# Optimization experiments

Measured on AMD Instinct MI355X. Metric: run time of the kernel, lower is better.

## Reference

```python
import jax, jax.numpy as jnp
import numpy as np

B, H, K, HID = 64, 32, 4096, 7168
Q_LORA, KV_LORA = 1536, 512
NOPE, ROPE, VDIM = 128, 64, 128
HEAD_SIZE = NOPE + ROPE  # 192
EPS = 1e-6
SOFTMAX_SCALE = HEAD_SIZE ** -0.5  # mscale = 1 (no yarn)


def rmsnorm(x, w, eps=EPS):
    return x * jax.lax.rsqrt(jnp.mean(x * x, axis=-1, keepdims=True) + eps) * w


def interleave_rope(x, cos, sin):
    # x: [..., ROPE]; replicate torch view(d//2,2).transpose(2,3).reshape(d):
    # interleaved [r0,i0,r1,i1,...] -> [r0,r1,...,i0,i1,...], then rotate-half RoPE.
    shp = x.shape
    x = jnp.swapaxes(x.reshape(shp[:-1] + (ROPE // 2, 2)), -1, -2).reshape(shp)
    x1, x2 = x[..., : ROPE // 2], x[..., ROPE // 2:]
    # cos/sin: [B, ROPE//2] -> broadcast over head axis
    c = cos[:, None, :]
    s = sin[:, None, :]
    return jnp.concatenate([x1 * c - x2 * s, x2 * c + x1 * s], axis=-1)


def setup_inputs() -> dict:
    key = jax.random.key(0)
    ks = jax.random.split(key, 12)
    w = 0.02
    return {
        "hidden_states": jax.random.normal(ks[0], (B, HID), jnp.float32),
        "cos": jax.random.uniform(ks[1], (B, ROPE // 2), jnp.float32),
        "sin": jax.random.uniform(ks[2], (B, ROPE // 2), jnp.float32),
        "kv_cache": jax.random.normal(ks[3], (B, K, KV_LORA + ROPE), jnp.float32),
        "w_q_a": jax.random.normal(ks[4], (HID, Q_LORA), jnp.float32) * w,
        "q_a_ln_w": jnp.ones((Q_LORA,), jnp.float32),
        "w_q_b": jax.random.normal(ks[5], (Q_LORA, H * HEAD_SIZE), jnp.float32) * w,
        "w_kv_a": jax.random.normal(ks[6], (HID, KV_LORA + ROPE), jnp.float32) * w,
        "kv_a_ln_w": jnp.ones((KV_LORA,), jnp.float32),
        "w_uk_t": jax.random.normal(ks[7], (H, NOPE, KV_LORA), jnp.float32) * w,
        "w_uv": jax.random.normal(ks[8], (H, KV_LORA, VDIM), jnp.float32) * w,
        "w_o": jax.random.normal(ks[9], (H * VDIM, HID), jnp.float32) * w,
        "slots": jnp.full((B,), K - 1, jnp.int32),
        "seq_lens": jnp.full((B,), K, jnp.int32),
    }


def reference(hidden_states, cos, sin, kv_cache, w_q_a, q_a_ln_w, w_q_b,
              w_kv_a, kv_a_ln_w, w_uk_t, w_uv, w_o, slots, seq_lens):
    # --- Q low-rank path: q_a_proj -> RMSNorm -> q_b_proj ---
    q_c = rmsnorm(hidden_states @ w_q_a, q_a_ln_w)          # [B, Q_LORA]
    q = (q_c @ w_q_b).reshape(B, H, HEAD_SIZE)              # [B, H, 192]
    q_nope, q_pe = q[..., :NOPE], q[..., NOPE:]

    # --- K-up absorption: ql_nope = q_nope @ W_UK_T (per head) ---
    ql_nope = jnp.einsum("bhn,hnr->bhr", q_nope, w_uk_t)    # [B, H, KV_LORA]

    # --- compressed KV projection ---
    ckv = hidden_states @ w_kv_a                            # [B, KV_LORA+ROPE]
    kv_c, k_pe = ckv[:, :KV_LORA], ckv[:, KV_LORA:]
    kv_c = rmsnorm(kv_c, kv_a_ln_w)                         # [B, KV_LORA]
    k_pe = k_pe[:, None, :]                                 # [B, 1, ROPE]

    # --- interleaved RoPE on pe parts ---
    q_pe = interleave_rope(q_pe, cos, sin)                  # [B, H, ROPE]
    k_pe = interleave_rope(k_pe, cos, sin)[:, 0, :]         # [B, ROPE]

    # --- latent cache writeback ---
    latent_k = jnp.concatenate([kv_c, k_pe], axis=-1)       # [B, KV_LORA+ROPE]
    cache = kv_cache.at[jnp.arange(B), slots].set(latent_k)  # [B, K, 576]

    # --- MLA latent attention (decode) ---
    query = jnp.concatenate([ql_nope, q_pe], axis=-1)       # [B, H, 576]
    scores = jnp.einsum("bhd,bkd->bhk", query, cache) * SOFTMAX_SCALE
    valid = (jnp.arange(K)[None, :] < seq_lens[:, None])[:, None, :]  # [B,1,K]
    scores = jnp.where(valid, scores, jnp.finfo(scores.dtype).min)
    probs = jax.nn.softmax(scores, axis=-1)                 # [B, H, K]
    attn = jnp.einsum("bhk,bkr->bhr", probs, cache[..., :KV_LORA])  # [B,H,KV_LORA]

    # --- V-up absorption + output projection ---
    out = jnp.einsum("bhr,hrv->bhv", attn, w_uv)            # [B, H, VDIM]
    return out.reshape(B, H * VDIM) @ w_o                   # [B, HID]
```

## Files before the change

### kernel.cpp

```cpp
#include <hip/hip_runtime.h>
#include <stdint.h>

#define NB 64
#define NH 32
#define KCTX 4096
#define HID 7168
#define QLORA 1536
#define KVL 512
#define DTOT 576
#define NSPLIT 4
#define KSPAN 1024
#define NTILE 64
#define TK 16
#define SM_SCALE 0.07216878364870323f
#define NEGINF (-3.0e38f)

typedef __attribute__((ext_vector_type(4))) float f32x4;
typedef __attribute__((ext_vector_type(8))) __bf16 bf16x8;

#define LGKM_BARRIER() do{ asm volatile("s_waitcnt lgkmcnt(0)" ::: "memory"); __builtin_amdgcn_s_barrier(); } while(0)

static __device__ __forceinline__ void glds16(const void* g, void* s){
    __builtin_amdgcn_global_load_lds((const __attribute__((address_space(1))) void*)g,
                                     (__attribute__((address_space(3))) void*)s, 16, 0, 0);
}

static __device__ __forceinline__ unsigned short f2bf(float f){
    union{__bf16 h; unsigned short s;} x; x.h = (__bf16)f; return x.s;
}
static __device__ __forceinline__ float bf2f(unsigned short h){
    union{unsigned i;float f;}x; x.i=((unsigned)h)<<16; return x.f;
}
static __device__ __forceinline__ unsigned pack2(float a, float b){
    union{__bf16 h[2]; unsigned u;} x; x.h[0]=(__bf16)a; x.h[1]=(__bf16)b; return x.u;
}

__global__ __launch_bounds__(256) void pack_a(const float* __restrict__ A,
        unsigned short* __restrict__ Hi, unsigned short* __restrict__ Lo, int K)
{
    int idx = blockIdx.x*256 + threadIdx.x;
    int m = idx & 63, kb = idx >> 6;
    const float* src = A + (size_t)m*K + kb*8;
    float v[8];
    *(float4*)(v)   = *(const float4*)(src);
    *(float4*)(v+4) = *(const float4*)(src+4);
    unsigned short h[8], l[8];
#pragma unroll
    for (int j=0;j<8;++j){
        h[j] = f2bf(v[j]);
        l[j] = f2bf(v[j] - bf2f(h[j]));
    }
    uint4 uh, ul;
    uh.x=(unsigned)h[0]|((unsigned)h[1]<<16); uh.y=(unsigned)h[2]|((unsigned)h[3]<<16);
    uh.z=(unsigned)h[4]|((unsigned)h[5]<<16); uh.w=(unsigned)h[6]|((unsigned)h[7]<<16);
    ul.x=(unsigned)l[0]|((unsigned)l[1]<<16); ul.y=(unsigned)l[2]|((unsigned)l[3]<<16);
    ul.z=(unsigned)l[4]|((unsigned)l[5]<<16); ul.w=(unsigned)l[6]|((unsigned)l[7]<<16);
    *(uint4*)(Hi + (size_t)idx*8) = uh;
    *(uint4*)(Lo + (size_t)idx*8) = ul;
}

static __device__ __forceinline__ void gemm_core(
        const unsigned short* __restrict__ Ahi, const unsigned short* __restrict__ Alo,
        const float* __restrict__ Wm, float* __restrict__ P, int N, int ksteps,
        int bx, int by,
        unsigned short* Ah, unsigned short* Al, unsigned short* Bh, unsigned short* Bl)
{
    const int tid = threadIdx.x;
    const int w = tid>>6, l = tid&63, lm = l&15, lg = l>>4;
    const int n0 = bx*64;
    const int s  = by;
    const int mn = tid&63, ks = tid>>6;
    const int widx = ((mn>>4)*64 + ks*16 + (mn&15));

    f32x4 acc[4];
#pragma unroll
    for (int i=0;i<4;++i){ acc[i][0]=0.f; acc[i][1]=0.f; acc[i][2]=0.f; acc[i][3]=0.f; }

    uint4 ah4, al4; float wv[8];
    auto load_raw = [&](int t){
        const int k0 = (s*ksteps + t)*32;
        size_t gidx = (size_t)((k0>>3) + ks)*64 + mn;
        ah4 = *(const uint4*)(Ahi + gidx*8);
        al4 = *(const uint4*)(Alo + gidx*8);
        const float* wp = Wm + (size_t)(k0 + ks*8)*N + n0 + mn;
#pragma unroll
        for (int j=0;j<8;++j) wv[j] = wp[(size_t)j*N];
    };
    auto cvt_write = [&](int buf){
        unsigned short h[8], lo[8];
#pragma unroll
        for (int j=0;j<8;++j){
            h[j]  = f2bf(wv[j]);
            lo[j] = f2bf(wv[j] - bf2f(h[j]));
        }
        uint4 bh4, bl4;
        bh4.x=(unsigned)h[0]|((unsigned)h[1]<<16); bh4.y=(unsigned)h[2]|((unsigned)h[3]<<16);
        bh4.z=(unsigned)h[4]|((unsigned)h[5]<<16); bh4.w=(unsigned)h[6]|((unsigned)h[7]<<16);
        bl4.x=(unsigned)lo[0]|((unsigned)lo[1]<<16); bl4.y=(unsigned)lo[2]|((unsigned)lo[3]<<16);
        bl4.z=(unsigned)lo[4]|((unsigned)lo[5]<<16); bl4.w=(unsigned)lo[6]|((unsigned)lo[7]<<16);
        *(uint4*)(Ah + buf*2048 + widx*8) = ah4;
        *(uint4*)(Al + buf*2048 + widx*8) = al4;
        *(uint4*)(Bh + buf*2048 + widx*8) = bh4;
        *(uint4*)(Bl + buf*2048 + widx*8) = bl4;
    };

    load_raw(0);
    for (int t=0; t<ksteps; ++t){
        const int buf = t&1;
        cvt_write(buf);
        __syncthreads();
        if (t+1 < ksteps) load_raw(t+1);
        const int fa = buf*2048 + (w*64 + lg*16 + lm)*8;
        bf16x8 fah = *(const bf16x8*)(Ah + fa);
        bf16x8 fal = *(const bf16x8*)(Al + fa);
#pragma unroll
        for (int nt=0;nt<4;++nt){
            const int fb = buf*2048 + (nt*64 + lg*16 + lm)*8;
            bf16x8 fbh = *(const bf16x8*)(Bh + fb);
            bf16x8 fbl = *(const bf16x8*)(Bl + fb);
            acc[nt] = __builtin_amdgcn_mfma_f32_16x16x32_bf16(fah, fbh, acc[nt], 0,0,0);
            acc[nt] = __builtin_amdgcn_mfma_f32_16x16x32_bf16(fal, fbh, acc[nt], 0,0,0);
            acc[nt] = __builtin_amdgcn_mfma_f32_16x16x32_bf16(fah, fbl, acc[nt], 0,0,0);
        }
        __syncthreads();
    }
#pragma unroll
    for (int nt=0;nt<4;++nt){
        int n = n0 + nt*16 + lm;
#pragma unroll
        for (int r=0;r<4;++r){
            int m = w*16 + lg*4 + r;
            P[((size_t)s*64 + m)*N + n] = acc[nt][r];
        }
    }
}

__global__ __launch_bounds__(256) void gemm_mfma(
        const unsigned short* __restrict__ Ahi, const unsigned short* __restrict__ Alo,
        const float* __restrict__ Wm, float* __restrict__ P, int N, int ksteps)
{
    __shared__ unsigned short Ah[2*2048], Al[2*2048], Bh[2*2048], Bl[2*2048];
    gemm_core(Ahi, Alo, Wm, P, N, ksteps, blockIdx.x, blockIdx.y, Ah, Al, Bh, Bl);
}

__global__ __launch_bounds__(256) void gemm_dual(
        const unsigned short* __restrict__ Ahi, const unsigned short* __restrict__ Alo,
        const float* __restrict__ W0, float* __restrict__ P0, int N0, int ks0, int nbx0, int nblk0,
        const float* __restrict__ W1, float* __restrict__ P1, int N1, int ks1, int nbx1)
{
    __shared__ unsigned short Ah[2*2048], Al[2*2048], Bh[2*2048], Bl[2*2048];
    int bid = blockIdx.x;
    if (bid < nblk0){
        gemm_core(Ahi, Alo, W0, P0, N0, ks0, bid%nbx0, bid/nbx0, Ah, Al, Bh, Bl);
    } else {
        bid -= nblk0;
        gemm_core(Ahi, Alo, W1, P1, N1, ks1, bid%nbx1, bid/nbx1, Ah, Al, Bh, Bl);
    }
}

static __device__ __forceinline__ void rms_core(const float* __restrict__ P,
        const float* __restrict__ w, unsigned short* __restrict__ Hi,
        unsigned short* __restrict__ Lo, int S, int b, float* red)
{
    const int t = threadIdx.x;
    float v[6]; float ss = 0.f;
#pragma unroll
    for (int j=0;j<6;++j){
        int n = j*256 + t;
        float s = 0.f;
        for (int sp=0; sp<S; ++sp) s += P[((size_t)sp*64+b)*1536 + n];
        v[j] = s; ss += s*s;
    }
#pragma unroll
    for (int off=32; off>=1; off>>=1) ss += __shfl_xor(ss, off, 64);
    if ((t&63)==0) red[t>>6] = ss;
    __syncthreads();
    float tot = red[0]+red[1]+red[2]+red[3];
    float rs = rsqrtf(tot/1536.f + 1e-6f);
#pragma unroll
    for (int j=0;j<6;++j){
        int n = j*256+t;
        float val = v[j]*rs*w[n];
        unsigned short hs = f2bf(val);
        unsigned short ls = f2bf(val - bf2f(hs));
        size_t ui = (size_t)(n>>3)*512 + b*8 + (n&7);
        Hi[ui] = hs; Lo[ui] = ls;
    }
}

static __device__ __forceinline__ void kvrope_core(const float* __restrict__ P,
        const float* __restrict__ w, const float* __restrict__ cosb, const float* __restrict__ sinb,
        float* __restrict__ latent, int S, int b, float* vals, float* red)
{
    const int t = threadIdx.x;
    float ss = 0.f;
    for (int j=0;j<3;++j){
        int n = j*256+t;
        if (n < 576){
            float s=0.f;
            for (int sp=0;sp<S;++sp) s += P[((size_t)sp*64+b)*576 + n];
            vals[n]=s;
            if (n<512) ss += s*s;
        }
    }
#pragma unroll
    for (int off=32; off>=1; off>>=1) ss += __shfl_xor(ss, off, 64);
    if ((t&63)==0) red[t>>6]=ss;
    __syncthreads();
    float tot = red[0]+red[1]+red[2]+red[3];
    float rs = rsqrtf(tot/512.f + 1e-6f);
    for (int j=0;j<3;++j){
        int n = j*256+t;
        if (n<576){
            float o;
            if (n < 512) o = vals[n]*rs*w[n];
            else if (n < 544){ int i=n-512; o = vals[512+2*i]*cosb[b*32+i] - vals[513+2*i]*sinb[b*32+i]; }
            else            { int i=n-544; o = vals[513+2*i]*cosb[b*32+i] + vals[512+2*i]*sinb[b*32+i]; }
            latent[(size_t)b*576 + n] = o;
        }
    }
}

__global__ __launch_bounds__(256) void norm_dual(
        const float* __restrict__ Pq, const float* __restrict__ qw,
        unsigned short* __restrict__ Hi, unsigned short* __restrict__ Lo, int Sq,
        const float* __restrict__ Pkv, const float* __restrict__ kvw,
        const float* __restrict__ cosb, const float* __restrict__ sinb,
        float* __restrict__ latent, int Skv)
{
    __shared__ float vals[576];
    __shared__ float red[4];
    if (blockIdx.x < 64) rms_core(Pq, qw, Hi, Lo, Sq, blockIdx.x, red);
    else                 kvrope_core(Pkv, kvw, cosb, sinb, latent, Skv, blockIdx.x-64, vals, red);
}

__global__ __launch_bounds__(256) void reduce_sum(const float* __restrict__ P,
        float* __restrict__ out, int S, int N)
{
    int i = blockIdx.x*256 + threadIdx.x;
    int b = i / N, n = i - b*N;
    float s = 0.f;
    for (int sp=0; sp<S; ++sp) s += P[((size_t)sp*64+b)*N + n];
    out[i] = s;
}

__global__ __launch_bounds__(256) void finish_q(const float* __restrict__ P,
        const float* __restrict__ cosb, const float* __restrict__ sinb,
        float* __restrict__ q, float* __restrict__ query, int S)
{
    int i = blockIdx.x*256 + threadIdx.x;
    int b = i / 6144, n = i - b*6144;
    float s = 0.f;
    for (int sp=0; sp<S; ++sp) s += P[((size_t)sp*64+b)*6144 + n];
    int h = n/192, nl = n - h*192;
    if (nl < 128){
        q[((size_t)b*32+h)*192 + nl] = s;
    } else {
        int i2 = (nl-128)>>1;
        float other = __shfl_xor(s, 1);
        float c = cosb[b*32+i2], sn = sinb[b*32+i2];
        float* o = query + ((size_t)b*32+h)*576;
        if ((nl&1)==0) o[512+i2] = s*c - other*sn;
        else           o[544+i2] = s*c + other*sn;
    }
}

__global__ __launch_bounds__(256) void qlnope_mfma(const float* __restrict__ q,
        const float* __restrict__ wukt, float* __restrict__ query)
{
    __shared__ unsigned short Bh[4096], Bl[4096];
    const int h = blockIdx.x, r0 = blockIdx.y*128;
    const int tid = threadIdx.x;
    const int w = tid>>6, l = tid&63, lm = l&15, lg = l>>4;
    f32x4 acc[8];
#pragma unroll
    for (int i=0;i<8;++i){ acc[i][0]=0.f; acc[i][1]=0.f; acc[i][2]=0.f; acc[i][3]=0.f; }

    for (int ck=0; ck<4; ++ck){
        const int k0 = ck*32;
        unsigned short hh[2][8], ll[2][8]; int wid0 = tid*2;
#pragma unroll
        for (int wi=0; wi<2; ++wi){
            int wid = wid0 + wi;
            int ntile = wid>>6, kg = (wid>>4)&3, nl = wid&15;
            int n = r0 + ntile*16 + nl;
            const float* wp = wukt + (size_t)h*65536 + (size_t)(k0+kg*8)*512 + n;
#pragma unroll
            for (int j=0;j<8;++j){
                float v = wp[(size_t)j*512];
                hh[wi][j] = f2bf(v);
                ll[wi][j] = f2bf(v - bf2f(hh[wi][j]));
            }
        }
        __syncthreads();
#pragma unroll
        for (int wi=0; wi<2; ++wi){
            int wid = wid0 + wi;
            uint4 uh, ul;
            uh.x=(unsigned)hh[wi][0]|((unsigned)hh[wi][1]<<16); uh.y=(unsigned)hh[wi][2]|((unsigned)hh[wi][3]<<16);
            uh.z=(unsigned)hh[wi][4]|((unsigned)hh[wi][5]<<16); uh.w=(unsigned)hh[wi][6]|((unsigned)hh[wi][7]<<16);
            ul.x=(unsigned)ll[wi][0]|((unsigned)ll[wi][1]<<16); ul.y=(unsigned)ll[wi][2]|((unsigned)ll[wi][3]<<16);
            ul.z=(unsigned)ll[wi][4]|((unsigned)ll[wi][5]<<16); ul.w=(unsigned)ll[wi][6]|((unsigned)ll[wi][7]<<16);
            *(uint4*)(Bh + wid*8) = uh;
            *(uint4*)(Bl + wid*8) = ul;
        }
        __syncthreads();
        const int bb = w*16 + lm;
        const float* ap = q + ((size_t)bb*32 + h)*192 + k0 + lg*8;
        float4 a0 = *(const float4*)ap;
        float4 a1 = *(const float4*)(ap+4);
        union{uint4 u; bf16x8 v;} fh, fl;
        fh.u.x=pack2(a0.x,a0.y); fh.u.y=pack2(a0.z,a0.w);
        fh.u.z=pack2(a1.x,a1.y); fh.u.w=pack2(a1.z,a1.w);
        float r0f=a0.x-bf2f(f2bf(a0.x)), r1f=a0.y-bf2f(f2bf(a0.y));
        float r2f=a0.z-bf2f(f2bf(a0.z)), r3f=a0.w-bf2f(f2bf(a0.w));
        float r4f=a1.x-bf2f(f2bf(a1.x)), r5f=a1.y-bf2f(f2bf(a1.y));
        float r6f=a1.z-bf2f(f2bf(a1.z)), r7f=a1.w-bf2f(f2bf(a1.w));
        fl.u.x=pack2(r0f,r1f); fl.u.y=pack2(r2f,r3f);
        fl.u.z=pack2(r4f,r5f); fl.u.w=pack2(r6f,r7f);
#pragma unroll
        for (int nt=0;nt<8;++nt){
            const int fb = (nt*64 + lg*16 + lm)*8;
            bf16x8 fbh = *(const bf16x8*)(Bh + fb);
            bf16x8 fbl = *(const bf16x8*)(Bl + fb);
            acc[nt] = __builtin_amdgcn_mfma_f32_16x16x32_bf16(fh.v, fbh, acc[nt], 0,0,0);
            acc[nt] = __builtin_amdgcn_mfma_f32_16x16x32_bf16(fl.v, fbh, acc[nt], 0,0,0);
            acc[nt] = __builtin_amdgcn_mfma_f32_16x16x32_bf16(fh.v, fbl, acc[nt], 0,0,0);
        }
        __syncthreads();
    }
#pragma unroll
    for (int nt=0;nt<8;++nt){
        int r = r0 + nt*16 + lm;
#pragma unroll
        for (int qq=0;qq<4;++qq){
            int bb = w*16 + lg*4 + qq;
            query[((size_t)bb*32 + h)*576 + r] = acc[nt][qq];
        }
    }
}

static __device__ __forceinline__ int vt_addr(int d, int key){
    return (d>>2)*64 + (((d&3)^((d>>3)&3))<<4) + key;
}

__global__ __launch_bounds__(512,1) void attn_mfma(const float* __restrict__ query,
        const float* __restrict__ kv, const float* __restrict__ latent,
        const int* __restrict__ slots, const int* __restrict__ seq_lens,
        float* __restrict__ Opart, float* __restrict__ Mpart, float* __restrict__ Lpart)
{
    __shared__ float Kf[3][16*576];
    __shared__ unsigned short Vt[8192];
    __shared__ float S_s[4][32][16];
    __shared__ unsigned short P_s[32][40];
    __shared__ float alpha_s[32];

    const int b = blockIdx.y, sp = blockIdx.x;
    const int tid = threadIdx.x;
    const int w = tid>>6, l = tid&63;
    const int lm = l&15, lg = l>>4;
    const int ht = w&1;
    const int dg = w>>1;
    const int cs = dg*5 - (dg>0?1:0);
    const int cnt = (dg==1||dg==2)?5:4;
    const int seqlen = seq_lens[b];
    const int slot = slots[b];
    const int k0 = sp*KSPAN;
    const int myh = tid>>4, s5 = tid&15;

    P_s[tid>>4][16 + (tid&15)] = 0;

    bf16x8 qf[5];
    {
        const float* qrow = query + ((size_t)b*32 + ht*16 + lm)*576;
#pragma unroll
        for (int ss=0;ss<5;++ss){
            if (ss < cnt){
                int d0 = (cs+ss)*32 + lg*8;
                float4 a = *(const float4*)(qrow + d0);
                float4 c = *(const float4*)(qrow + d0 + 4);
                union{uint4 u; bf16x8 v;} cv;
                cv.u.x=pack2(a.x,a.y); cv.u.y=pack2(a.z,a.w);
                cv.u.z=pack2(c.x,c.y); cv.u.w=pack2(c.z,c.w);
                qf[ss]=cv.v;
            } else {
                union{uint4 u; bf16x8 v;} z; z.u.x=0; z.u.y=0; z.u.z=0; z.u.w=0;
                qf[ss]=z.v;
            }
        }
    }

    auto issue_tile = [&](int tt, int buf){
        const int gkb = k0 + tt*TK;
#pragma unroll
        for (int i=0;i<5;++i){
            int s = i*8 + w;
            if (s < 36){
                int B = s*1024 + l*16;
                int r = B / 2304;
                int gs = (B - r*2304) >> 4;
                int g  = gs ^ (r&7);
                int gk = gkb + r; if (gk > KCTX-1) gk = KCTX-1;
                const float* src = (gk==slot) ? (latent + (size_t)b*576 + g*4)
                                              : (kv + ((size_t)b*KCTX + gk)*576 + g*4);
                glds16(src, ((char*)&Kf[buf][0]) + B);
            }
        }
    };

    f32x4 oacc[8];
#pragma unroll
    for (int i=0;i<8;++i){ oacc[i][0]=0.f; oacc[i][1]=0.f; oacc[i][2]=0.f; oacc[i][3]=0.f; }
    float m_run = NEGINF, l_run = 0.f;

    issue_tile(0, 0);
    issue_tile(1, 1);
    if (w < 4) { asm volatile("s_waitcnt vmcnt(5)" ::: "memory"); }
    else       { asm volatile("s_waitcnt vmcnt(4)" ::: "memory"); }
    __builtin_amdgcn_s_barrier();

    int cur = 0;
    for (int tt=0; tt<NTILE; ++tt){
        if (tt+2 < NTILE){
            int ib = cur+2; if (ib>=3) ib-=3;
            issue_tile(tt+2, ib);
        }

        {
            const int kg = tid&1;
            const int dq = (tid>>1)&127;
            const int rep = tid>>8;
            float4 rv[4];
#pragma unroll
            for (int i=0;i<4;++i){
                int r = kg*8 + rep*4 + i;
                rv[i] = *(const float4*)(&Kf[cur][r*576 + ((dq ^ (r&7))<<2)]);
            }
#pragma unroll
            for (int j=0;j<4;++j){
                uint2 o;
                o.x = pack2(((const float*)&rv[0])[j], ((const float*)&rv[1])[j]);
                o.y = pack2(((const float*)&rv[2])[j], ((const float*)&rv[3])[j]);
                *(uint2*)(Vt + vt_addr(dq*4+j, kg*8) + rep*4) = o;
            }
        }
        {
            f32x4 sacc; sacc[0]=0.f; sacc[1]=0.f; sacc[2]=0.f; sacc[3]=0.f;
            const float* kb = &Kf[cur][lm*576];
            const int sw = lm&7;
            __builtin_amdgcn_s_setprio(1);
#pragma unroll
            for (int ss=0;ss<5;++ss){
                int chunk = cs + (ss<cnt ? ss : 0);
                int g = chunk*8 + lg*2;
                float4 fa = *(const float4*)(kb + ((g ^ sw)<<2));
                float4 fb = *(const float4*)(kb + (((g+1) ^ sw)<<2));
                union{uint4 u; bf16x8 v;} cv;
                cv.u.x = pack2(fa.x, fa.y); cv.u.y = pack2(fa.z, fa.w);
                cv.u.z = pack2(fb.x, fb.y); cv.u.w = pack2(fb.z, fb.w);
                sacc = __builtin_amdgcn_mfma_f32_16x16x32_bf16(qf[ss], cv.v, sacc, 0,0,0);
            }
            __builtin_amdgcn_s_setprio(0);
#pragma unroll
            for (int r=0;r<4;++r) S_s[dg][ht*16 + (lg<<2) + r][lm] = sacc[r];
        }
        LGKM_BARRIER();

        {
            const int kbase = k0 + tt*TK;
            float v = (S_s[0][myh][s5] + S_s[1][myh][s5]
                     + S_s[2][myh][s5] + S_s[3][myh][s5])*SM_SCALE;
            float sc = (kbase + s5 < seqlen) ? v : NEGINF;
            float tmax = sc;
            tmax = fmaxf(tmax, __shfl_xor(tmax,1));
            tmax = fmaxf(tmax, __shfl_xor(tmax,2));
            tmax = fmaxf(tmax, __shfl_xor(tmax,4));
            tmax = fmaxf(tmax, __shfl_xor(tmax,8));
            float mnew = fmaxf(m_run, tmax);
            float al = __expf(m_run - mnew);
            float pv = (sc > 0.5f*NEGINF) ? __expf(sc-mnew) : 0.f;
            P_s[myh][s5] = f2bf(pv);
            float ps = pv;
            ps += __shfl_xor(ps,1); ps += __shfl_xor(ps,2);
            ps += __shfl_xor(ps,4); ps += __shfl_xor(ps,8);
            l_run = l_run*al + ps;
            m_run = mnew;
            if (s5==0) alpha_s[myh] = al;
        }
        LGKM_BARRIER();

        {
            float al4[4];
#pragma unroll
            for (int r=0;r<4;++r) al4[r] = alpha_s[ht*16 + (lg<<2) + r];
            bf16x8 pa = *(const bf16x8*)(&P_s[ht*16+lm][lg*8]);
            __builtin_amdgcn_s_setprio(1);
#pragma unroll
            for (int nt=0;nt<8;++nt){
                f32x4 o = oacc[nt];
                o[0]*=al4[0]; o[1]*=al4[1]; o[2]*=al4[2]; o[3]*=al4[3];
                int r = dg*128 + nt*16 + lm;
                bf16x8 bv = *(const bf16x8*)(Vt + vt_addr(r, (lg&1)*8));
                oacc[nt] = __builtin_amdgcn_mfma_f32_16x16x32_bf16(pa, bv, o, 0,0,0);
            }
            __builtin_amdgcn_s_setprio(0);
        }
        if (tt+2 < NTILE){
            if (w < 4) { asm volatile("s_waitcnt vmcnt(5)" ::: "memory"); }
            else       { asm volatile("s_waitcnt vmcnt(4)" ::: "memory"); }
            __builtin_amdgcn_s_barrier();
        } else if (tt+1 < NTILE){
            asm volatile("s_waitcnt vmcnt(0)" ::: "memory");
            __builtin_amdgcn_s_barrier();
        }
        cur = cur+1; if (cur>=3) cur-=3;
    }

    const int obase = (b*NSPLIT+sp)*32;
#pragma unroll
    for (int nt=0;nt<8;++nt){
        int r = dg*128 + nt*16 + lm;
#pragma unroll
        for (int qq=0;qq<4;++qq){
            int h = ht*16 + (lg<<2) + qq;
            Opart[((size_t)(obase+h))*512 + r] = oacc[nt][qq];
        }
    }
    if (s5==0){ Mpart[obase+myh]=m_run; Lpart[obase+myh]=l_run; }
}

__global__ __launch_bounds__(256) void av_uv_merge(const float* __restrict__ Opart,
        const float* __restrict__ Mpart, const float* __restrict__ Lpart,
        const float* __restrict__ wuv,
        unsigned short* __restrict__ Hi, unsigned short* __restrict__ Lo)
{
    __shared__ unsigned short Bh[4096], Bl[4096];
    __shared__ unsigned short Ah[512], Al[512];
    __shared__ float lwn[16][4];
    const int h = blockIdx.x, bg = blockIdx.y;
    const int tid = threadIdx.x;
    const int w = tid>>6, l = tid&63, lm = l&15, lg = l>>4;

    if (tid < 16){
        int b = bg*16 + tid;
        float m0 = Mpart[(b*NSPLIT+0)*32+h], m1 = Mpart[(b*NSPLIT+1)*32+h];
        float m2 = Mpart[(b*NSPLIT+2)*32+h], m3 = Mpart[(b*NSPLIT+3)*32+h];
        float M = fmaxf(fmaxf(m0,m1),fmaxf(m2,m3));
        float w0 = __expf(m0-M), w1 = __expf(m1-M), w2 = __expf(m2-M), w3 = __expf(m3-M);
        float L = w0*Lpart[(b*NSPLIT+0)*32+h] + w1*Lpart[(b*NSPLIT+1)*32+h]
                + w2*Lpart[(b*NSPLIT+2)*32+h] + w3*Lpart[(b*NSPLIT+3)*32+h];
        float inv = 1.f/L;
        lwn[tid][0]=w0*inv; lwn[tid][1]=w1*inv; lwn[tid][2]=w2*inv; lwn[tid][3]=w3*inv;
    }
    __syncthreads();

    f32x4 acc[2];
#pragma unroll
    for (int i=0;i<2;++i){ acc[i][0]=0.f; acc[i][1]=0.f; acc[i][2]=0.f; acc[i][3]=0.f; }

    for (int ck=0; ck<16; ++ck){
        const int k0 = ck*32;
        unsigned short hh[2][8], ll[2][8]; int wid0 = tid*2;
#pragma unroll
        for (int wi=0; wi<2; ++wi){
            int wid = wid0 + wi;
            int ntile = wid>>6, kg = (wid>>4)&3, nl = wid&15;
            int n = ntile*16 + nl;
            const float* wp = wuv + (size_t)h*65536 + (size_t)(k0+kg*8)*128 + n;
#pragma unroll
            for (int j=0;j<8;++j){
                float v = wp[(size_t)j*128];
                hh[wi][j] = f2bf(v);
                ll[wi][j] = f2bf(v - bf2f(hh[wi][j]));
            }
        }
        float av[2];
#pragma unroll
        for (int e=0;e<2;++e){
            int id = tid*2+e;
            int row = id>>5, k = id&31;
            int bb = bg*16 + row;
            const float* op = Opart + (((size_t)bb*NSPLIT)*32 + h)*512 + k0 + k;
            av[e] = lwn[row][0]*op[0] + lwn[row][1]*op[16384]
                  + lwn[row][2]*op[32768] + lwn[row][3]*op[49152];
        }
        __syncthreads();
#pragma unroll
        for (int wi=0; wi<2; ++wi){
            int wid = wid0 + wi;
            uint4 uh, ul;
            uh.x=(unsigned)hh[wi][0]|((unsigned)hh[wi][1]<<16); uh.y=(unsigned)hh[wi][2]|((unsigned)hh[wi][3]<<16);
            uh.z=(unsigned)hh[wi][4]|((unsigned)hh[wi][5]<<16); uh.w=(unsigned)hh[wi][6]|((unsigned)hh[wi][7]<<16);
            ul.x=(unsigned)ll[wi][0]|((unsigned)ll[wi][1]<<16); ul.y=(unsigned)ll[wi][2]|((unsigned)ll[wi][3]<<16);
            ul.z=(unsigned)ll[wi][4]|((unsigned)ll[wi][5]<<16); ul.w=(unsigned)ll[wi][6]|((unsigned)ll[wi][7]<<16);
            *(uint4*)(Bh + wid*8) = uh;
            *(uint4*)(Bl + wid*8) = ul;
        }
#pragma unroll
        for (int e=0;e<2;++e){
            int id = tid*2+e;
            int row = id>>5, k = id&31;
            unsigned short hs = f2bf(av[e]);
            unsigned short ls = f2bf(av[e] - bf2f(hs));
            int ai = ((k>>3)*16 + row)*8 + (k&7);
            Ah[ai] = hs; Al[ai] = ls;
        }
        __syncthreads();
        const int fa = (lg*16 + lm)*8;
        bf16x8 fah = *(const bf16x8*)(Ah + fa);
        bf16x8 fal = *(const bf16x8*)(Al + fa);
#pragma unroll
        for (int i=0;i<2;++i){
            int nt = w*2 + i;
            const int fb = (nt*64 + lg*16 + lm)*8;
            bf16x8 fbh = *(const bf16x8*)(Bh + fb);
            bf16x8 fbl = *(const bf16x8*)(Bl + fb);
            acc[i] = __builtin_amdgcn_mfma_f32_16x16x32_bf16(fah, fbh, acc[i], 0,0,0);
            acc[i] = __builtin_amdgcn_mfma_f32_16x16x32_bf16(fal, fbh, acc[i], 0,0,0);
            acc[i] = __builtin_amdgcn_mfma_f32_16x16x32_bf16(fah, fbl, acc[i], 0,0,0);
        }
        __syncthreads();
    }
#pragma unroll
    for (int i=0;i<2;++i){
        int nt = w*2 + i;
#pragma unroll
        for (int qq=0;qq<4;++qq){
            float val = acc[i][qq];
            int bb = bg*16 + lg*4 + qq;
            int k = h*128 + nt*16 + lm;
            unsigned short hv = f2bf(val);
            unsigned short lv = f2bf(val - bf2f(hv));
            size_t ui = (size_t)(k>>3)*512 + bb*8 + (k&7);
            Hi[ui] = hv; Lo[ui] = lv;
        }
    }
}

extern "C" void kernel_launch(void* const* d_in, const int* in_sizes, int n_in,
                              void* d_out, int out_size, void* d_ws, size_t ws_size,
                              hipStream_t stream)
{
    const float* hidden = (const float*)d_in[0];
    const float* cosb   = (const float*)d_in[1];
    const float* sinb   = (const float*)d_in[2];
    const float* kv     = (const float*)d_in[3];
    const float* w_q_a  = (const float*)d_in[4];
    const float* q_ln   = (const float*)d_in[5];
    const float* w_q_b  = (const float*)d_in[6];
    const float* w_kv_a = (const float*)d_in[7];
    const float* kv_ln  = (const float*)d_in[8];
    const float* w_uk_t = (const float*)d_in[9];
    const float* w_uv   = (const float*)d_in[10];
    const float* w_o    = (const float*)d_in[11];
    const int* slots    = (const int*)d_in[12];
    const int* seqlens  = (const int*)d_in[13];
    float* out = (float*)d_out;

    float* W = (float*)d_ws;
    float* P0     = W;
    float* P1     = W + 4194304;
    float* q      = W + 6291456;
    float* query  = W + 6684672;
    float* latent = W + 7864320;
    float* Mp     = W + 7901184;
    float* Lp     = W + 7909376;
    unsigned short* pkhid_h = (unsigned short*)(W + 7917568);
    unsigned short* pkhid_l = (unsigned short*)(W + 8146944);
    unsigned short* pkqc_h  = (unsigned short*)(W + 8376320);
    unsigned short* pkqc_l  = (unsigned short*)(W + 8425472);
    unsigned short* pkao_h  = (unsigned short*)(W + 8474624);
    unsigned short* pkao_l  = (unsigned short*)(W + 8605696);

    hipLaunchKernelGGL(pack_a, dim3(224), dim3(256), 0, stream, hidden, pkhid_h, pkhid_l, 7168);
    hipLaunchKernelGGL(gemm_dual, dim3(672+504), dim3(256), 0, stream,
                       pkhid_h, pkhid_l, w_q_a, P0, 1536, 8, 24, 672, w_kv_a, P1, 576, 4, 9);
    hipLaunchKernelGGL(norm_dual, dim3(128), dim3(256), 0, stream,
                       P0, q_ln, pkqc_h, pkqc_l, 28, P1, kv_ln, cosb, sinb, latent, 56);
    hipLaunchKernelGGL(gemm_mfma, dim3(96,6), dim3(256), 0, stream, pkqc_h, pkqc_l, w_q_b, P0, 6144, 8);
    hipLaunchKernelGGL(finish_q, dim3(1536), dim3(256), 0, stream, P0, cosb, sinb, q, query, 6);
    hipLaunchKernelGGL(qlnope_mfma, dim3(32,4), dim3(256), 0, stream, q, w_uk_t, query);
    hipLaunchKernelGGL(attn_mfma, dim3(NSPLIT,64), dim3(512), 0, stream,
                       query, kv, latent, slots, seqlens, P0, Mp, Lp);
    hipLaunchKernelGGL(av_uv_merge, dim3(32,4), dim3(256), 0, stream, P0, Mp, Lp, w_uv, pkao_h, pkao_l);
    hipLaunchKernelGGL(gemm_mfma, dim3(112,8), dim3(256), 0, stream, pkao_h, pkao_l, w_o, P0, 7168, 16);
    hipLaunchKernelGGL(reduce_sum, dim3(1792), dim3(256), 0, stream, P0, out, 8, 7168);
}
```

Baseline: 332.6 us.

## Fuse A-packing into GEMMs, atomic output reduction, repartition attention score waves

Removes the separate pack_a kernel by converting the fp32 hidden states to hi/lo bf16 inside the first dual GEMM. The final split-K GEMM now atomically adds into a zeroed output instead of running a reduce_sum kernel. finish_q writes q directly as pre-split bf16 hi/lo in MFMA-friendly layout, so qlnope skips conversion. The attention score stage is repartitioned so each of the 8 waves covers both head tiles over 2-3 chunks, with an 8-way shared-memory reduction. Fewer launches and less intermediate traffic, at the cost of atomics (nondeterministic sum order) and a memset.

```diff
diff --git a/kernel.cpp b/kernel.cpp
--- a/kernel.cpp
+++ b/kernel.cpp
@@ -35,31 +35,8 @@
     union{__bf16 h[2]; unsigned u;} x; x.h[0]=(__bf16)a; x.h[1]=(__bf16)b; return x.u;
 }
 
-__global__ __launch_bounds__(256) void pack_a(const float* __restrict__ A,
-        unsigned short* __restrict__ Hi, unsigned short* __restrict__ Lo, int K)
-{
-    int idx = blockIdx.x*256 + threadIdx.x;
-    int m = idx & 63, kb = idx >> 6;
-    const float* src = A + (size_t)m*K + kb*8;
-    float v[8];
-    *(float4*)(v)   = *(const float4*)(src);
-    *(float4*)(v+4) = *(const float4*)(src+4);
-    unsigned short h[8], l[8];
-#pragma unroll
-    for (int j=0;j<8;++j){
-        h[j] = f2bf(v[j]);
-        l[j] = f2bf(v[j] - bf2f(h[j]));
-    }
-    uint4 uh, ul;
-    uh.x=(unsigned)h[0]|((unsigned)h[1]<<16); uh.y=(unsigned)h[2]|((unsigned)h[3]<<16);
-    uh.z=(unsigned)h[4]|((unsigned)h[5]<<16); uh.w=(unsigned)h[6]|((unsigned)h[7]<<16);
-    ul.x=(unsigned)l[0]|((unsigned)l[1]<<16); ul.y=(unsigned)l[2]|((unsigned)l[3]<<16);
-    ul.z=(unsigned)l[4]|((unsigned)l[5]<<16); ul.w=(unsigned)l[6]|((unsigned)l[7]<<16);
-    *(uint4*)(Hi + (size_t)idx*8) = uh;
-    *(uint4*)(Lo + (size_t)idx*8) = ul;
-}
-
-static __device__ __forceinline__ void gemm_core(
+template<int OUT_MODE>
+static __device__ __forceinline__ void gemm_core_packed(
         const unsigned short* __restrict__ Ahi, const unsigned short* __restrict__ Alo,
         const float* __restrict__ Wm, float* __restrict__ P, int N, int ksteps,
         int bx, int by,
@@ -87,17 +64,17 @@
         for (int j=0;j<8;++j) wv[j] = wp[(size_t)j*N];
     };
     auto cvt_write = [&](int buf){
-        unsigned short h[8], lo[8];
+        unsigned short h8[8], l8[8];
 #pragma unroll
         for (int j=0;j<8;++j){
-            h[j]  = f2bf(wv[j]);
-            lo[j] = f2bf(wv[j] - bf2f(h[j]));
+            h8[j] = f2bf(wv[j]);
+            l8[j] = f2bf(wv[j] - bf2f(h8[j]));
         }
         uint4 bh4, bl4;
-        bh4.x=(unsigned)h[0]|((unsigned)h[1]<<16); bh4.y=(unsigned)h[2]|((unsigned)h[3]<<16);
-        bh4.z=(unsigned)h[4]|((unsigned)h[5]<<16); bh4.w=(unsigned)h[6]|((unsigned)h[7]<<16);
-        bl4.x=(unsigned)lo[0]|((unsigned)lo[1]<<16); bl4.y=(unsigned)lo[2]|((unsigned)lo[3]<<16);
-        bl4.z=(unsigned)lo[4]|((unsigned)lo[5]<<16); bl4.w=(unsigned)lo[6]|((unsigned)lo[7]<<16);
+        bh4.x=(unsigned)h8[0]|((unsigned)h8[1]<<16); bh4.y=(unsigned)h8[2]|((unsigned)h8[3]<<16);
+        bh4.z=(unsigned)h8[4]|((unsigned)h8[5]<<16); bh4.w=(unsigned)h8[6]|((unsigned)h8[7]<<16);
+        bl4.x=(unsigned)l8[0]|((unsigned)l8[1]<<16); bl4.y=(unsigned)l8[2]|((unsigned)l8[3]<<16);
+        bl4.z=(unsigned)l8[4]|((unsigned)l8[5]<<16); bl4.w=(unsigned)l8[6]|((unsigned)l8[7]<<16);
         *(uint4*)(Ah + buf*2048 + widx*8) = ah4;
         *(uint4*)(Al + buf*2048 + widx*8) = al4;
         *(uint4*)(Bh + buf*2048 + widx*8) = bh4;
@@ -130,6 +107,87 @@
 #pragma unroll
         for (int r=0;r<4;++r){
             int m = w*16 + lg*4 + r;
+            if (OUT_MODE == 0) P[((size_t)s*64 + m)*N + n] = acc[nt][r];
+            else               unsafeAtomicAdd(&P[(size_t)m*N + n], acc[nt][r]);
+        }
+    }
+}
+
+static __device__ __forceinline__ void gemm_core_raw(
+        const float* __restrict__ Araw, int KA,
+        const float* __restrict__ Wm, float* __restrict__ P, int N, int ksteps,
+        int bx, int by,
+        unsigned short* Ah, unsigned short* Al, unsigned short* Bh, unsigned short* Bl)
+{
+    const int tid = threadIdx.x;
+    const int w = tid>>6, l = tid&63, lm = l&15, lg = l>>4;
+    const int n0 = bx*64;
+    const int s  = by;
+    const int mn = tid&63, ks = tid>>6;
+    const int widx = ((mn>>4)*64 + ks*16 + (mn&15));
+
+    f32x4 acc[4];
+#pragma unroll
+    for (int i=0;i<4;++i){ acc[i][0]=0.f; acc[i][1]=0.f; acc[i][2]=0.f; acc[i][3]=0.f; }
+
+    float av[8], wv[8];
+    auto load_raw = [&](int t){
+        const int k0 = (s*ksteps + t)*32;
+        const float* ap = Araw + (size_t)mn*KA + k0 + ks*8;
+        *(float4*)(av)   = *(const float4*)(ap);
+        *(float4*)(av+4) = *(const float4*)(ap+4);
+        const float* wp = Wm + (size_t)(k0 + ks*8)*N + n0 + mn;
+#pragma unroll
+        for (int j=0;j<8;++j) wv[j] = wp[(size_t)j*N];
+    };
+    auto cvt_write = [&](int buf){
+        unsigned short ha[8], la[8], hb[8], lb[8];
+#pragma unroll
+        for (int j=0;j<8;++j){
+            ha[j] = f2bf(av[j]); la[j] = f2bf(av[j] - bf2f(ha[j]));
+            hb[j] = f2bf(wv[j]); lb[j] = f2bf(wv[j] - bf2f(hb[j]));
+        }
+        uint4 ah4, al4, bh4, bl4;
+        ah4.x=(unsigned)ha[0]|((unsigned)ha[1]<<16); ah4.y=(unsigned)ha[2]|((unsigned)ha[3]<<16);
+        ah4.z=(unsigned)ha[4]|((unsigned)ha[5]<<16); ah4.w=(unsigned)ha[6]|((unsigned)ha[7]<<16);
+        al4.x=(unsigned)la[0]|((unsigned)la[1]<<16); al4.y=(unsigned)la[2]|((unsigned)la[3]<<16);
+        al4.z=(unsigned)la[4]|((unsigned)la[5]<<16); al4.w=(unsigned)la[6]|((unsigned)la[7]<<16);
+        bh4.x=(unsigned)hb[0]|((unsigned)hb[1]<<16); bh4.y=(unsigned)hb[2]|((unsigned)hb[3]<<16);
+        bh4.z=(unsigned)hb[4]|((unsigned)hb[5]<<16); bh4.w=(unsigned)hb[6]|((unsigned)hb[7]<<16);
+        bl4.x=(unsigned)lb[0]|((unsigned)lb[1]<<16); bl4.y=(unsigned)lb[2]|((unsigned)lb[3]<<16);
+        bl4.z=(unsigned)lb[4]|((unsigned)lb[5]<<16); bl4.w=(unsigned)lb[6]|((unsigned)lb[7]<<16);
+        *(uint4*)(Ah + buf*2048 + widx*8) = ah4;
+        *(uint4*)(Al + buf*2048 + widx*8) = al4;
+        *(uint4*)(Bh + buf*2048 + widx*8) = bh4;
+        *(uint4*)(Bl + buf*2048 + widx*8) = bl4;
+    };
+
+    load_raw(0);
+    for (int t=0; t<ksteps; ++t){
+        const int buf = t&1;
+        cvt_write(buf);
+        __syncthreads();
+        if (t+1 < ksteps) load_raw(t+1);
+        const int fa = buf*2048 + (w*64 + lg*16 + lm)*8;
+        bf16x8 fah = *(const bf16x8*)(Ah + fa);
+        bf16x8 fal = *(const bf16x8*)(Al + fa);
+#pragma unroll
+        for (int nt=0;nt<4;++nt){
+            const int fb = buf*2048 + (nt*64 + lg*16 + lm)*8;
+            bf16x8 fbh = *(const bf16x8*)(Bh + fb);
+            bf16x8 fbl = *(const bf16x8*)(Bl + fb);
+            acc[nt] = __builtin_amdgcn_mfma_f32_16x16x32_bf16(fah, fbh, acc[nt], 0,0,0);
+            acc[nt] = __builtin_amdgcn_mfma_f32_16x16x32_bf16(fal, fbh, acc[nt], 0,0,0);
+            acc[nt] = __builtin_amdgcn_mfma_f32_16x16x32_bf16(fah, fbl, acc[nt], 0,0,0);
+        }
+        __syncthreads();
+    }
+#pragma unroll
+    for (int nt=0;nt<4;++nt){
+        int n = n0 + nt*16 + lm;
+#pragma unroll
+        for (int r=0;r<4;++r){
+            int m = w*16 + lg*4 + r;
             P[((size_t)s*64 + m)*N + n] = acc[nt][r];
         }
     }
@@ -140,21 +198,29 @@
         const float* __restrict__ Wm, float* __restrict__ P, int N, int ksteps)
 {
     __shared__ unsigned short Ah[2*2048], Al[2*2048], Bh[2*2048], Bl[2*2048];
-    gemm_core(Ahi, Alo, Wm, P, N, ksteps, blockIdx.x, blockIdx.y, Ah, Al, Bh, Bl);
-}
-
-__global__ __launch_bounds__(256) void gemm_dual(
+    gemm_core_packed<0>(Ahi, Alo, Wm, P, N, ksteps, blockIdx.x, blockIdx.y, Ah, Al, Bh, Bl);
+}
+
+__global__ __launch_bounds__(256) void gemm_atomic(
         const unsigned short* __restrict__ Ahi, const unsigned short* __restrict__ Alo,
+        const float* __restrict__ Wm, float* __restrict__ Out, int N, int ksteps)
+{
+    __shared__ unsigned short Ah[2*2048], Al[2*2048], Bh[2*2048], Bl[2*2048];
+    gemm_core_packed<1>(Ahi, Alo, Wm, Out, N, ksteps, blockIdx.x, blockIdx.y, Ah, Al, Bh, Bl);
+}
+
+__global__ __launch_bounds__(256) void gemm_dual_raw(
+        const float* __restrict__ Araw, int KA,
         const float* __restrict__ W0, float* __restrict__ P0, int N0, int ks0, int nbx0, int nblk0,
         const float* __restrict__ W1, float* __restrict__ P1, int N1, int ks1, int nbx1)
 {
     __shared__ unsigned short Ah[2*2048], Al[2*2048], Bh[2*2048], Bl[2*2048];
     int bid = blockIdx.x;
     if (bid < nblk0){
-        gemm_core(Ahi, Alo, W0, P0, N0, ks0, bid%nbx0, bid/nbx0, Ah, Al, Bh, Bl);
+        gemm_core_raw(Araw, KA, W0, P0, N0, ks0, bid%nbx0, bid/nbx0, Ah, Al, Bh, Bl);
     } else {
         bid -= nblk0;
-        gemm_core(Ahi, Alo, W1, P1, N1, ks1, bid%nbx1, bid/nbx1, Ah, Al, Bh, Bl);
+        gemm_core_raw(Araw, KA, W1, P1, N1, ks1, bid%nbx1, bid/nbx1, Ah, Al, Bh, Bl);
     }
 }
 
@@ -234,19 +300,10 @@
     else                 kvrope_core(Pkv, kvw, cosb, sinb, latent, Skv, blockIdx.x-64, vals, red);
 }
 
-__global__ __launch_bounds__(256) void reduce_sum(const float* __restrict__ P,
-        float* __restrict__ out, int S, int N)
-{
-    int i = blockIdx.x*256 + threadIdx.x;
-    int b = i / N, n = i - b*N;
-    float s = 0.f;
-    for (int sp=0; sp<S; ++sp) s += P[((size_t)sp*64+b)*N + n];
-    out[i] = s;
-}
-
 __global__ __launch_bounds__(256) void finish_q(const float* __restrict__ P,
         const float* __restrict__ cosb, const float* __restrict__ sinb,
-        float* __restrict__ q, float* __restrict__ query, int S)
+        unsigned short* __restrict__ qh, unsigned short* __restrict__ ql,
+        float* __restrict__ query, int S)
 {
     int i = blockIdx.x*256 + threadIdx.x;
     int b = i / 6144, n = i - b*6144;
@@ -254,7 +311,10 @@
     for (int sp=0; sp<S; ++sp) s += P[((size_t)sp*64+b)*6144 + n];
     int h = n/192, nl = n - h*192;
     if (nl < 128){
-        q[((size_t)b*32+h)*192 + nl] = s;
+        unsigned short hs = f2bf(s);
+        unsigned short ls = f2bf(s - bf2f(hs));
+        size_t ui = (size_t)h*8192 + (size_t)(nl>>3)*512 + b*8 + (nl&7);
+        qh[ui]=hs; ql[ui]=ls;
     } else {
         int i2 = (nl-128)>>1;
         float other = __shfl_xor(s, 1);
@@ -265,7 +325,8 @@
     }
 }
 
-__global__ __launch_bounds__(256) void qlnope_mfma(const float* __restrict__ q,
+__global__ __launch_bounds__(256) void qlnope_mfma(const unsigned short* __restrict__ qh,
+        const unsigned short* __restrict__ ql,
         const float* __restrict__ wukt, float* __restrict__ query)
 {
     __shared__ unsigned short Bh[4096], Bl[4096];
@@ -305,19 +366,10 @@
             *(uint4*)(Bl + wid*8) = ul;
         }
         __syncthreads();
-        const int bb = w*16 + lm;
-        const float* ap = q + ((size_t)bb*32 + h)*192 + k0 + lg*8;
-        float4 a0 = *(const float4*)ap;
-        float4 a1 = *(const float4*)(ap+4);
+        size_t ai = (size_t)h*8192 + (size_t)(ck*4+lg)*512 + (size_t)(w*16+lm)*8;
         union{uint4 u; bf16x8 v;} fh, fl;
-        fh.u.x=pack2(a0.x,a0.y); fh.u.y=pack2(a0.z,a0.w);
-        fh.u.z=pack2(a1.x,a1.y); fh.u.w=pack2(a1.z,a1.w);
-        float r0f=a0.x-bf2f(f2bf(a0.x)), r1f=a0.y-bf2f(f2bf(a0.y));
-        float r2f=a0.z-bf2f(f2bf(a0.z)), r3f=a0.w-bf2f(f2bf(a0.w));
-        float r4f=a1.x-bf2f(f2bf(a1.x)), r5f=a1.y-bf2f(f2bf(a1.y));
-        float r6f=a1.z-bf2f(f2bf(a1.z)), r7f=a1.w-bf2f(f2bf(a1.w));
-        fl.u.x=pack2(r0f,r1f); fl.u.y=pack2(r2f,r3f);
-        fl.u.z=pack2(r4f,r5f); fl.u.w=pack2(r6f,r7f);
+        fh.u = *(const uint4*)(qh + ai);
+        fl.u = *(const uint4*)(ql + ai);
 #pragma unroll
         for (int nt=0;nt<8;++nt){
             const int fb = (nt*64 + lg*16 + lm)*8;
@@ -351,7 +403,7 @@
 {
     __shared__ float Kf[3][16*576];
     __shared__ unsigned short Vt[8192];
-    __shared__ float S_s[4][32][16];
+    __shared__ float S_s[8][32][16];
     __shared__ unsigned short P_s[32][40];
     __shared__ float alpha_s[32];
 
@@ -361,8 +413,8 @@
     const int lm = l&15, lg = l>>4;
     const int ht = w&1;
     const int dg = w>>1;
-    const int cs = dg*5 - (dg>0?1:0);
-    const int cnt = (dg==1||dg==2)?5:4;
+    const int cs = 2*w + (w>=1?1:0) + (w>=5?1:0);
+    const int cnt = ((w&3)==0)?3:2;
     const int seqlen = seq_lens[b];
     const int slot = slots[b];
     const int k0 = sp*KSPAN;
@@ -370,23 +422,23 @@
 
     P_s[tid>>4][16 + (tid&15)] = 0;
 
-    bf16x8 qf[5];
-    {
-        const float* qrow = query + ((size_t)b*32 + ht*16 + lm)*576;
-#pragma unroll
-        for (int ss=0;ss<5;++ss){
+    bf16x8 qf[2][3];
+#pragma unroll
+    for (int h2=0; h2<2; ++h2){
+        const float* qrow = query + ((size_t)b*32 + h2*16 + lm)*576;
+#pragma unroll
+        for (int ss=0;ss<3;++ss){
+            union{uint4 u; bf16x8 v;} cv;
             if (ss < cnt){
                 int d0 = (cs+ss)*32 + lg*8;
                 float4 a = *(const float4*)(qrow + d0);
                 float4 c = *(const float4*)(qrow + d0 + 4);
-                union{uint4 u; bf16x8 v;} cv;
                 cv.u.x=pack2(a.x,a.y); cv.u.y=pack2(a.z,a.w);
                 cv.u.z=pack2(c.x,c.y); cv.u.w=pack2(c.z,c.w);
-                qf[ss]=cv.v;
             } else {
-                union{uint4 u; bf16x8 v;} z; z.u.x=0; z.u.y=0; z.u.z=0; z.u.w=0;
-                qf[ss]=z.v;
-            }
+                cv.u.x=0; cv.u.y=0; cv.u.z=0; cv.u.w=0;
+            }
+            qf[h2][ss]=cv.v;
         }
     }
 
@@ -445,31 +497,40 @@
             }
         }
         {
-            f32x4 sacc; sacc[0]=0.f; sacc[1]=0.f; sacc[2]=0.f; sacc[3]=0.f;
+            f32x4 s0, s1;
+            s0[0]=0.f; s0[1]=0.f; s0[2]=0.f; s0[3]=0.f;
+            s1[0]=0.f; s1[1]=0.f; s1[2]=0.f; s1[3]=0.f;
             const float* kb = &Kf[cur][lm*576];
             const int sw = lm&7;
             __builtin_amdgcn_s_setprio(1);
 #pragma unroll
-            for (int ss=0;ss<5;++ss){
-                int chunk = cs + (ss<cnt ? ss : 0);
-                int g = chunk*8 + lg*2;
-                float4 fa = *(const float4*)(kb + ((g ^ sw)<<2));
-                float4 fb = *(const float4*)(kb + (((g+1) ^ sw)<<2));
-                union{uint4 u; bf16x8 v;} cv;
-                cv.u.x = pack2(fa.x, fa.y); cv.u.y = pack2(fa.z, fa.w);
-                cv.u.z = pack2(fb.x, fb.y); cv.u.w = pack2(fb.z, fb.w);
-                sacc = __builtin_amdgcn_mfma_f32_16x16x32_bf16(qf[ss], cv.v, sacc, 0,0,0);
+            for (int ss=0;ss<3;++ss){
+                if (ss < cnt){
+                    int g = (cs+ss)*8 + lg*2;
+                    float4 fa = *(const float4*)(kb + ((g ^ sw)<<2));
+                    float4 fb = *(const float4*)(kb + (((g+1) ^ sw)<<2));
+                    union{uint4 u; bf16x8 v;} cv;
+                    cv.u.x = pack2(fa.x, fa.y); cv.u.y = pack2(fa.z, fa.w);
+                    cv.u.z = pack2(fb.x, fb.y); cv.u.w = pack2(fb.z, fb.w);
+                    s0 = __builtin_amdgcn_mfma_f32_16x16x32_bf16(qf[0][ss], cv.v, s0, 0,0,0);
+                    s1 = __builtin_amdgcn_mfma_f32_16x16x32_bf16(qf[1][ss], cv.v, s1, 0,0,0);
+                }
             }
             __builtin_amdgcn_s_setprio(0);
 #pragma unroll
-            for (int r=0;r<4;++r) S_s[dg][ht*16 + (lg<<2) + r][lm] = sacc[r];
+            for (int r=0;r<4;++r){
+                S_s[w][(lg<<2)+r][lm]      = s0[r];
+                S_s[w][16+(lg<<2)+r][lm]   = s1[r];
+            }
         }
         LGKM_BARRIER();
 
         {
             const int kbase = k0 + tt*TK;
-            float v = (S_s[0][myh][s5] + S_s[1][myh][s5]
-                     + S_s[2][myh][s5] + S_s[3][myh][s5])*SM_SCALE;
+            float v = 0.f;
+#pragma unroll
+            for (int i=0;i<8;++i) v += S_s[i][myh][s5];
+            v *= SM_SCALE;
             float sc = (kbase + s5 < seqlen) ? v : NEGINF;
             float tmax = sc;
             tmax = fmaxf(tmax, __shfl_xor(tmax,1));
@@ -660,29 +721,28 @@
     float* W = (float*)d_ws;
     float* P0     = W;
     float* P1     = W + 4194304;
-    float* q      = W + 6291456;
-    float* query  = W + 6684672;
-    float* latent = W + 7864320;
-    float* Mp     = W + 7901184;
-    float* Lp     = W + 7909376;
-    unsigned short* pkhid_h = (unsigned short*)(W + 7917568);
-    unsigned short* pkhid_l = (unsigned short*)(W + 8146944);
-    unsigned short* pkqc_h  = (unsigned short*)(W + 8376320);
-    unsigned short* pkqc_l  = (unsigned short*)(W + 8425472);
-    unsigned short* pkao_h  = (unsigned short*)(W + 8474624);
-    unsigned short* pkao_l  = (unsigned short*)(W + 8605696);
-
-    hipLaunchKernelGGL(pack_a, dim3(224), dim3(256), 0, stream, hidden, pkhid_h, pkhid_l, 7168);
-    hipLaunchKernelGGL(gemm_dual, dim3(672+504), dim3(256), 0, stream,
-                       pkhid_h, pkhid_l, w_q_a, P0, 1536, 8, 24, 672, w_kv_a, P1, 576, 4, 9);
+    float* query  = W + 6291456;
+    float* latent = W + 7471104;
+    float* Mp     = W + 7507968;
+    float* Lp     = W + 7516160;
+    unsigned short* pkq_h  = (unsigned short*)(W + 7524352);
+    unsigned short* pkq_l  = (unsigned short*)(W + 7655424);
+    unsigned short* pkqc_h = (unsigned short*)(W + 7786496);
+    unsigned short* pkqc_l = (unsigned short*)(W + 7835648);
+    unsigned short* pkao_h = (unsigned short*)(W + 7884800);
+    unsigned short* pkao_l = (unsigned short*)(W + 8015872);
+
+    hipMemsetAsync(out, 0, (size_t)NB*HID*sizeof(float), stream);
+
+    hipLaunchKernelGGL(gemm_dual_raw, dim3(672+504), dim3(256), 0, stream,
+                       hidden, HID, w_q_a, P0, 1536, 8, 24, 672, w_kv_a, P1, 576, 4, 9);
     hipLaunchKernelGGL(norm_dual, dim3(128), dim3(256), 0, stream,
                        P0, q_ln, pkqc_h, pkqc_l, 28, P1, kv_ln, cosb, sinb, latent, 56);
     hipLaunchKernelGGL(gemm_mfma, dim3(96,6), dim3(256), 0, stream, pkqc_h, pkqc_l, w_q_b, P0, 6144, 8);
-    hipLaunchKernelGGL(finish_q, dim3(1536), dim3(256), 0, stream, P0, cosb, sinb, q, query, 6);
-    hipLaunchKernelGGL(qlnope_mfma, dim3(32,4), dim3(256), 0, stream, q, w_uk_t, query);
+    hipLaunchKernelGGL(finish_q, dim3(1536), dim3(256), 0, stream, P0, cosb, sinb, pkq_h, pkq_l, query, 6);
+    hipLaunchKernelGGL(qlnope_mfma, dim3(32,4), dim3(256), 0, stream, pkq_h, pkq_l, w_uk_t, query);
     hipLaunchKernelGGL(attn_mfma, dim3(NSPLIT,64), dim3(512), 0, stream,
                        query, kv, latent, slots, seqlens, P0, Mp, Lp);
     hipLaunchKernelGGL(av_uv_merge, dim3(32,4), dim3(256), 0, stream, P0, Mp, Lp, w_uv, pkao_h, pkao_l);
-    hipLaunchKernelGGL(gemm_mfma, dim3(112,8), dim3(256), 0, stream, pkao_h, pkao_l, w_o, P0, 7168, 16);
-    hipLaunchKernelGGL(reduce_sum, dim3(1792), dim3(256), 0, stream, P0, out, 8, 7168);
-}
+    hipLaunchKernelGGL(gemm_atomic, dim3(112,8), dim3(256), 0, stream, pkao_h, pkao_l, w_o, out, 7168, 16);
+}
```

After: 330.2 us. About the same (-0.7%).
